# Kernel optimization log

Hardware: AMD Instinct MI355X
Metric: run time of the kernel (lower is better)

Reference implementation:

```python
import jax, jax.numpy as jnp
import numpy as np


def setup_inputs() -> dict:
    key = jax.random.key(0)
    k1, k2, k3 = jax.random.split(key, 3)
    b, n, h, d = 2, 2048, 16, 64
    q = jax.random.normal(k1, (b, n, h, d), dtype=jnp.float32)
    k = jax.random.normal(k2, (b, n, h, d), dtype=jnp.float32)
    v = jax.random.normal(k3, (b, n, h, d), dtype=jnp.float32)
    return {"q": q, "k": k, "v": v, "is_causal": 1}


def reference(q, k, v, is_causal):
    # q, k, v: [b, n, h, d]
    b, n, h, d = q.shape
    scale = 1.0 / jnp.sqrt(jnp.asarray(d, dtype=q.dtype))
    # scores: [b, h, n_q, n_k]
    scores = jnp.einsum("bqhd,bkhd->bhqk", q, k) * scale
    if is_causal:
        causal_mask = jnp.triu(jnp.ones((n, n), dtype=bool), k=1)  # True above diagonal
        scores = jnp.where(causal_mask[None, None, :, :], jnp.asarray(-jnp.inf, scores.dtype), scores)
    attn = jax.nn.softmax(scores, axis=-1)
    # output back to [b, n, h, d]
    out = jnp.einsum("bhqk,bkhd->bqhd", attn, v)
    return out
```

## Files before the change

### kernel.cpp

```cpp
#include <hip/hip_runtime.h>
#include <hip/hip_bf16.h>
#include <math.h>

typedef __bf16 bf16x8 __attribute__((ext_vector_type(8)));
typedef __bf16 bf16x4 __attribute__((ext_vector_type(4)));
typedef __bf16 bf16x2 __attribute__((ext_vector_type(2)));
typedef float  f32x4  __attribute__((ext_vector_type(4)));
typedef float  f32x16 __attribute__((ext_vector_type(16)));
typedef unsigned int u32;
typedef unsigned int u32x4 __attribute__((ext_vector_type(4)));

#define HD   64
#define MNEG (-1e30f)
#define KSW(r, c) ((c) ^ (((r) & 7) << 3))
#define VSW(r, c) ((c) ^ ((((r) >> 2) & 7) << 3))

#define NSLOT   1024
#define ACC_FL  (NSLOT * 8192)
#define ML_FL   (NSLOT * 256)
#define WS_NEED ((size_t)(ACC_FL + ML_FL) * 4)

static __device__ __forceinline__ u32 pkbf(float a, float b) {
  bf16x2 t; t[0] = (__bf16)a; t[1] = (__bf16)b;
  return __builtin_bit_cast(u32, t);
}

template <int SPLIT>
__global__ __launch_bounds__(256, 2)
void fattn_fwd(const float* __restrict__ Q, const float* __restrict__ K,
               const float* __restrict__ V, const int* __restrict__ causal_p,
               float* __restrict__ O, float* __restrict__ wsAcc,
               float* __restrict__ wsML, int B, int N, int H) {
  __shared__ alignas(16) __bf16 Kl[2][64][64];
  __shared__ alignas(16) __bf16 Vt[2][64][64];

  const int tid  = threadIdx.x;
  const int wave = tid >> 6;
  const int lane = tid & 63;
  const int l31  = lane & 31;
  const int h    = lane >> 5;
  const int lo16 = lane & 15, hi4 = lane >> 4;

  const int causal = causal_p[0];

  int x, bh, t0, t1, slot = 0;
  if constexpr (SPLIT) {
    bh = (int)blockIdx.x & 31;
    const int xc = (int)blockIdx.x >> 5;
    x = 15 - (xc >> 1);
    const int c = xc & 1;
    const int ntile = causal ? (2 * x + 2) : 32;
    t0 = c * 16;
    t1 = min(t0 + 16, ntile);
    if (t0 >= t1) return;
    slot = (bh * 16 + x) * 2 + c;
  } else {
    x  = 15 - ((int)blockIdx.x >> 5);
    bh = (int)blockIdx.x & 31;
    t0 = 0;
    t1 = causal ? (2 * x + 2) : 32;
  }
  const int bb = bh / H, hh = bh - bb * H;
  const int sN = H * HD;

  const float* Qb = Q + (long)bb * N * sN + hh * HD;
  const float* Kb = K + (long)bb * N * sN + hh * HD;
  const float* Vb = V + (long)bb * N * sN + hh * HD;
  float*       Ob = O + (long)bb * N * sN + hh * HD;

  const int q0w = x * 128 + wave * 32;

  const float qscale = 0.125f * 1.44269504088896340736f;
  bf16x8 aq[4];
  {
    const float* qrow = Qb + (long)(q0w + l31) * sN;
#pragma unroll
    for (int ds = 0; ds < 4; ++ds) {
      f32x4 x0 = *(const f32x4*)(qrow + ds * 16 + h * 8);
      f32x4 x1 = *(const f32x4*)(qrow + ds * 16 + h * 8 + 4);
      bf16x8 a;
#pragma unroll
      for (int j = 0; j < 4; ++j) {
        a[j]     = (__bf16)(x0[j] * qscale);
        a[j + 4] = (__bf16)(x1[j] * qscale);
      }
      aq[ds] = a;
    }
  }

  f32x16 accA, accB;
#pragma unroll
  for (int j = 0; j < 16; ++j) { accA[j] = 0.f; accB[j] = 0.f; }
  float m_run = MNEG, l_run = 0.f;

  f32x4 kreg[4], vreg[4];
  auto issue = [&](int tt) {
    const int k0 = tt * 64;
#pragma unroll
    for (int i = 0; i < 4; ++i) {
      const int fl = tid + i * 256;
      const int r = fl >> 4, c4 = (fl & 15) * 4;
      kreg[i] = *(const f32x4*)(Kb + (long)(k0 + r) * sN + c4);
    }
    const float* vrow = Vb + (long)(k0 + wave * 16 + hi4 * 4) * sN + lo16 * 4;
#pragma unroll
    for (int q = 0; q < 4; ++q) vreg[q] = *(const f32x4*)(vrow + (long)q * sN);
  };
  auto wr = [&](int buf) {
#pragma unroll
    for (int i = 0; i < 4; ++i) {
      const int fl = tid + i * 256;
      const int r = fl >> 4, c4 = (fl & 15) * 4;
      bf16x4 kb;
#pragma unroll
      for (int j = 0; j < 4; ++j) kb[j] = (__bf16)kreg[i][j];
      *(bf16x4*)&Kl[buf][r][KSW(r, c4)] = kb;
    }
    const int kv0 = wave * 16 + hi4 * 4;
#pragma unroll
    for (int j = 0; j < 4; ++j) {
      const int d = lo16 * 4 + j;
      bf16x4 vv;
#pragma unroll
      for (int q = 0; q < 4; ++q) vv[q] = (__bf16)vreg[q][j];
      *(bf16x4*)&Vt[buf][d][VSW(d, kv0)] = vv;
    }
  };

  issue(t0);
  wr(0);
  __syncthreads();

  int pb = 0;
  for (int t = t0; t < t1; ++t) {
    const bool pf = (t + 1 < t1);
    if (pf) issue(t + 1);
    const int k0 = t * 64;

    f32x16 p0, p1;
#pragma unroll
    for (int j = 0; j < 16; ++j) { p0[j] = 0.f; p1[j] = 0.f; }
#pragma unroll
    for (int ds = 0; ds < 4; ++ds) {
      const int cc = ds * 16 + h * 8;
      bf16x8 ka = *(const bf16x8*)&Kl[pb][l31][KSW(l31, cc)];
      p0 = __builtin_amdgcn_mfma_f32_32x32x16_bf16(ka, aq[ds], p0, 0, 0, 0);
      bf16x8 kb2 = *(const bf16x8*)&Kl[pb][32 + l31][KSW(32 + l31, cc)];
      p1 = __builtin_amdgcn_mfma_f32_32x32x16_bf16(kb2, aq[ds], p1, 0, 0, 0);
    }

    if (causal && t >= 2 * x) {
      const int qg = q0w + l31;
#pragma unroll
      for (int reg = 0; reg < 16; ++reg) {
        const int crow = (reg & 3) + 8 * (reg >> 2) + 4 * h;
        if (k0 + crow > qg)      p0[reg] = MNEG;
        if (k0 + 32 + crow > qg) p1[reg] = MNEG;
      }
    }

    float t8[8];
#pragma unroll
    for (int j = 0; j < 8; ++j)
      t8[j] = fmaxf(fmaxf(p0[j], p0[j + 8]), fmaxf(p1[j], p1[j + 8]));
#pragma unroll
    for (int stp = 4; stp > 0; stp >>= 1)
#pragma unroll
      for (int j = 0; j < stp; ++j) t8[j] = fmaxf(t8[j], t8[j + stp]);
    const float mx = fmaxf(t8[0], __shfl_xor(t8[0], 32));
    if (!__all(mx - m_run <= 8.0f)) {
      const float mnew = fmaxf(m_run, mx);
      const float fac  = exp2f(m_run - mnew);
      l_run *= fac;
      m_run = mnew;
#pragma unroll
      for (int j = 0; j < 16; ++j) { accA[j] *= fac; accB[j] *= fac; }
    }
#pragma unroll
    for (int j = 0; j < 16; ++j) {
      p0[j] = exp2f(p0[j] - m_run);
      p1[j] = exp2f(p1[j] - m_run);
    }
    float s8[8];
#pragma unroll
    for (int j = 0; j < 8; ++j)
      s8[j] = (p0[j] + p0[j + 8]) + (p1[j] + p1[j + 8]);
#pragma unroll
    for (int stp = 4; stp > 0; stp >>= 1)
#pragma unroll
      for (int j = 0; j < stp; ++j) s8[j] += s8[j + stp];
    const float ps = s8[0] + __shfl_xor(s8[0], 32);
    l_run += ps;

    u32 W0[8], W1[8];
#pragma unroll
    for (int tt = 0; tt < 8; ++tt) {
      W0[tt] = pkbf(p0[2 * tt], p0[2 * tt + 1]);
      W1[tt] = pkbf(p1[2 * tt], p1[2 * tt + 1]);
    }
    auto mkpair = [&](u32 wa, u32 wb, u32& dlo, u32& dhi) {
      const u32 gsel = h ? wa : wb;
      const u32 f = (u32)__shfl_xor((int)gsel, 32);
      dlo = h ? f : wa;
      dhi = h ? wb : f;
    };
    bf16x8 pa[4];
    {
      u32 d0, d1, d2, d3;
      mkpair(W0[0], W0[2], d0, d2); mkpair(W0[1], W0[3], d1, d3);
      pa[0] = __builtin_bit_cast(bf16x8, (u32x4){d0, d1, d2, d3});
      mkpair(W0[4], W0[6], d0, d2); mkpair(W0[5], W0[7], d1, d3);
      pa[1] = __builtin_bit_cast(bf16x8, (u32x4){d0, d1, d2, d3});
      mkpair(W1[0], W1[2], d0, d2); mkpair(W1[1], W1[3], d1, d3);
      pa[2] = __builtin_bit_cast(bf16x8, (u32x4){d0, d1, d2, d3});
      mkpair(W1[4], W1[6], d0, d2); mkpair(W1[5], W1[7], d1, d3);
      pa[3] = __builtin_bit_cast(bf16x8, (u32x4){d0, d1, d2, d3});
    }

#pragma unroll
    for (int ks = 0; ks < 4; ++ks) {
      bf16x8 va = *(const bf16x8*)&Vt[pb][l31][VSW(l31, ks * 16 + h * 8)];
      accA = __builtin_amdgcn_mfma_f32_32x32x16_bf16(va, pa[ks], accA, 0, 0, 0);
    }
#pragma unroll
    for (int ks = 0; ks < 4; ++ks) {
      bf16x8 va = *(const bf16x8*)&Vt[pb][32 + l31][VSW(32 + l31, ks * 16 + h * 8)];
      accB = __builtin_amdgcn_mfma_f32_32x32x16_bf16(va, pa[ks], accB, 0, 0, 0);
    }

    if (pf) wr(pb ^ 1);
    __syncthreads();
    pb ^= 1;
  }

  const int qrel = wave * 32 + l31;
  if constexpr (SPLIT) {
    float* ap = wsAcc + (long)slot * 8192 + qrel * 64;
#pragma unroll
    for (int g = 0; g < 4; ++g) {
      f32x4 o0, o1;
#pragma unroll
      for (int j = 0; j < 4; ++j) { o0[j] = accA[4 * g + j]; o1[j] = accB[4 * g + j]; }
      *(f32x4*)(ap + 8 * g + 4 * h) = o0;
      *(f32x4*)(ap + 32 + 8 * g + 4 * h) = o1;
    }
    if (h == 0) {
      wsML[slot * 256 + qrel] = m_run;
      wsML[slot * 256 + 128 + qrel] = l_run;
    }
  } else {
    const float linv = 1.0f / l_run;
    float* orow = Ob + (long)(q0w + l31) * sN;
#pragma unroll
    for (int g = 0; g < 4; ++g) {
      f32x4 o0, o1;
#pragma unroll
      for (int j = 0; j < 4; ++j) {
        o0[j] = accA[4 * g + j] * linv;
        o1[j] = accB[4 * g + j] * linv;
      }
      *(f32x4*)(orow + 8 * g + 4 * h) = o0;
      *(f32x4*)(orow + 32 + 8 * g + 4 * h) = o1;
    }
  }
}

__global__ __launch_bounds__(256)
void fmerge(const float* __restrict__ wsAcc, const float* __restrict__ wsML,
            const int* __restrict__ causal_p, float* __restrict__ O,
            int B, int N, int H) {
  const int tid = threadIdx.x;
  const int bh = (int)blockIdx.x >> 4;
  const int x  = (int)blockIdx.x & 15;
  const int bb = bh / H, hh = bh - bb * H;
  const int causal = causal_p[0];
  const int ntile = causal ? (2 * x + 2) : 32;
  const int q  = tid >> 1;
  const int dh = (tid & 1) * 32;
  const int slot0 = (bh * 16 + x) * 2;
  const bool v1 = (16 < ntile);

  const float m0 = wsML[slot0 * 256 + q];
  const float l0 = wsML[slot0 * 256 + 128 + q];
  const float m1 = v1 ? wsML[(slot0 + 1) * 256 + q] : MNEG;
  const float l1 = v1 ? wsML[(slot0 + 1) * 256 + 128 + q] : 0.f;
  const float M  = fmaxf(m0, m1);
  const float e0 = exp2f(m0 - M);
  const float e1 = v1 ? exp2f(m1 - M) : 0.f;
  const float inv = 1.0f / (e0 * l0 + e1 * l1);
  const float f0 = e0 * inv, f1 = e1 * inv;

  const float* a0 = wsAcc + (long)slot0 * 8192 + q * 64 + dh;
  const float* a1 = a0 + 8192;
  float* op = O + ((long)(bb * N + x * 128 + q) * H + hh) * HD + dh;
#pragma unroll
  for (int j = 0; j < 8; ++j) {
    f32x4 r0 = *(const f32x4*)(a0 + 4 * j);
    f32x4 o;
#pragma unroll
    for (int e = 0; e < 4; ++e) o[e] = r0[e] * f0;
    if (v1) {
      f32x4 r1 = *(const f32x4*)(a1 + 4 * j);
#pragma unroll
      for (int e = 0; e < 4; ++e) o[e] += r1[e] * f1;
    }
    *(f32x4*)(op + 4 * j) = o;
  }
}

extern "C" void kernel_launch(void* const* d_in, const int* in_sizes, int n_in,
                              void* d_out, int out_size, void* d_ws, size_t ws_size,
                              hipStream_t stream) {
  const float* q = (const float*)d_in[0];
  const float* k = (const float*)d_in[1];
  const float* v = (const float*)d_in[2];
  const int* causal = (const int*)d_in[3];
  float* out = (float*)d_out;
  const int B = 2, N = 2048, H = 16;
  if (ws_size >= WS_NEED) {
    float* wsAcc = (float*)d_ws;
    float* wsML  = wsAcc + ACC_FL;
    fattn_fwd<1><<<dim3(NSLOT), dim3(256), 0, stream>>>(q, k, v, causal, out,
                                                        wsAcc, wsML, B, N, H);
    fmerge<<<dim3(512), dim3(256), 0, stream>>>(wsAcc, wsML, causal, out, B, N, H);
  } else {
    fattn_fwd<0><<<dim3(512), dim3(256), 0, stream>>>(q, k, v, causal, out,
                                                      nullptr, nullptr, B, N, H);
  }
}
```

Baseline: 162.2 us.

## Fuse split-KV merge into attention kernel via atomic counters, reorder and raise occupancy

Removes the separate merge kernel. The last-arriving split block, detected with an atomic counter per query tile, merges both partial results and writes the output directly. Query tiles that need only one chunk now write the output straight away, skipping the workspace round trip. Other changes in the same commit: a lookup table reorders block scheduling to pair long and short chunks, launch bounds rise to 4 blocks per SM, the MFMA sections are wrapped in s_setprio, and exp2f is replaced by the hardware exp2 builtin. The cost is a memset launch for the counters, extra fences, and possible register spilling under the tighter occupancy bound.

```diff
diff --git a/kernel.cpp b/kernel.cpp
--- a/kernel.cpp
+++ b/kernel.cpp
@@ -15,10 +15,24 @@
 #define KSW(r, c) ((c) ^ (((r) & 7) << 3))
 #define VSW(r, c) ((c) ^ ((((r) >> 2) & 7) << 3))
 
-#define NSLOT   1024
-#define ACC_FL  (NSLOT * 8192)
-#define ML_FL   (NSLOT * 256)
-#define WS_NEED ((size_t)(ACC_FL + ML_FL) * 4)
+#if __has_builtin(__builtin_amdgcn_exp2f)
+#define EXP2(x) __builtin_amdgcn_exp2f(x)
+#else
+#define EXP2(x) exp2f(x)
+#endif
+
+#define NSLOT    1024
+#define ACC_FL   (NSLOT * 8192)
+#define ML_FL    (NSLOT * 256)
+#define NCTR     512
+#define WS_NEED  ((size_t)(ACC_FL + ML_FL) * 4 + NCTR * 4)
+
+static __device__ const signed char ORD_X[32] =
+  {15,15,14,13,12,11,10,9,8,7, 14,6, 13,5, 12,4, 11,3, 10,2, 9,1, 8,0,
+   7,6,5,4,3,2,1,0};
+static __device__ const signed char ORD_C[32] =
+  {0,1,0,0,0,0,0,0,0,0, 1,0, 1,0, 1,0, 1,0, 1,0, 1,0, 1,0,
+   1,1,1,1,1,1,1,1};
 
 static __device__ __forceinline__ u32 pkbf(float a, float b) {
   bf16x2 t; t[0] = (__bf16)a; t[1] = (__bf16)b;
@@ -26,13 +40,15 @@
 }
 
 template <int SPLIT>
-__global__ __launch_bounds__(256, 2)
+__global__ __launch_bounds__(256, 4)
 void fattn_fwd(const float* __restrict__ Q, const float* __restrict__ K,
                const float* __restrict__ V, const int* __restrict__ causal_p,
                float* __restrict__ O, float* __restrict__ wsAcc,
-               float* __restrict__ wsML, int B, int N, int H) {
+               float* __restrict__ wsML, int* __restrict__ ctr,
+               int B, int N, int H) {
   __shared__ alignas(16) __bf16 Kl[2][64][64];
   __shared__ alignas(16) __bf16 Vt[2][64][64];
+  __shared__ int s_old;
 
   const int tid  = threadIdx.x;
   const int wave = tid >> 6;
@@ -43,16 +59,17 @@
 
   const int causal = causal_p[0];
 
-  int x, bh, t0, t1, slot = 0;
+  int x, bh, t0, t1, slot = 0, nch = 1;
   if constexpr (SPLIT) {
     bh = (int)blockIdx.x & 31;
-    const int xc = (int)blockIdx.x >> 5;
-    x = 15 - (xc >> 1);
-    const int c = xc & 1;
+    const int idx = (int)blockIdx.x >> 5;
+    x = ORD_X[idx];
+    const int c = ORD_C[idx];
     const int ntile = causal ? (2 * x + 2) : 32;
     t0 = c * 16;
     t1 = min(t0 + 16, ntile);
     if (t0 >= t1) return;
+    nch  = (ntile > 16) ? 2 : 1;
     slot = (bh * 16 + x) * 2 + c;
   } else {
     x  = 15 - ((int)blockIdx.x >> 5);
@@ -140,6 +157,7 @@
     f32x16 p0, p1;
 #pragma unroll
     for (int j = 0; j < 16; ++j) { p0[j] = 0.f; p1[j] = 0.f; }
+    __builtin_amdgcn_s_setprio(1);
 #pragma unroll
     for (int ds = 0; ds < 4; ++ds) {
       const int cc = ds * 16 + h * 8;
@@ -148,6 +166,7 @@
       bf16x8 kb2 = *(const bf16x8*)&Kl[pb][32 + l31][KSW(32 + l31, cc)];
       p1 = __builtin_amdgcn_mfma_f32_32x32x16_bf16(kb2, aq[ds], p1, 0, 0, 0);
     }
+    __builtin_amdgcn_s_setprio(0);
 
     if (causal && t >= 2 * x) {
       const int qg = q0w + l31;
@@ -170,7 +189,7 @@
     const float mx = fmaxf(t8[0], __shfl_xor(t8[0], 32));
     if (!__all(mx - m_run <= 8.0f)) {
       const float mnew = fmaxf(m_run, mx);
-      const float fac  = exp2f(m_run - mnew);
+      const float fac  = EXP2(m_run - mnew);
       l_run *= fac;
       m_run = mnew;
 #pragma unroll
@@ -178,8 +197,8 @@
     }
 #pragma unroll
     for (int j = 0; j < 16; ++j) {
-      p0[j] = exp2f(p0[j] - m_run);
-      p1[j] = exp2f(p1[j] - m_run);
+      p0[j] = EXP2(p0[j] - m_run);
+      p1[j] = EXP2(p1[j] - m_run);
     }
     float s8[8];
 #pragma unroll
@@ -217,6 +236,7 @@
       pa[3] = __builtin_bit_cast(bf16x8, (u32x4){d0, d1, d2, d3});
     }
 
+    __builtin_amdgcn_s_setprio(1);
 #pragma unroll
     for (int ks = 0; ks < 4; ++ks) {
       bf16x8 va = *(const bf16x8*)&Vt[pb][l31][VSW(l31, ks * 16 + h * 8)];
@@ -227,6 +247,7 @@
       bf16x8 va = *(const bf16x8*)&Vt[pb][32 + l31][VSW(32 + l31, ks * 16 + h * 8)];
       accB = __builtin_amdgcn_mfma_f32_32x32x16_bf16(va, pa[ks], accB, 0, 0, 0);
     }
+    __builtin_amdgcn_s_setprio(0);
 
     if (pf) wr(pb ^ 1);
     __syncthreads();
@@ -234,7 +255,7 @@
   }
 
   const int qrel = wave * 32 + l31;
-  if constexpr (SPLIT) {
+  if (SPLIT && nch == 2) {
     float* ap = wsAcc + (long)slot * 8192 + qrel * 64;
 #pragma unroll
     for (int g = 0; g < 4; ++g) {
@@ -247,6 +268,34 @@
     if (h == 0) {
       wsML[slot * 256 + qrel] = m_run;
       wsML[slot * 256 + 128 + qrel] = l_run;
+    }
+    __threadfence();
+    if (tid == 0) s_old = atomicAdd(&ctr[bh * 16 + x], 1);
+    __syncthreads();
+    if (s_old == 0) return;
+    __threadfence();
+    const int oslot = slot ^ 1;
+    const float mo  = wsML[oslot * 256 + qrel];
+    const float lo_ = wsML[oslot * 256 + 128 + qrel];
+    const float M   = fmaxf(m_run, mo);
+    const float e0  = EXP2(m_run - M);
+    const float e1  = EXP2(mo - M);
+    const float inv = 1.0f / (l_run * e0 + lo_ * e1);
+    const float f0 = e0 * inv, f1 = e1 * inv;
+    const float* bp = wsAcc + (long)oslot * 8192 + qrel * 64;
+    float* orow = Ob + (long)(q0w + l31) * sN;
+#pragma unroll
+    for (int g = 0; g < 4; ++g) {
+      f32x4 r0 = *(const f32x4*)(bp + 8 * g + 4 * h);
+      f32x4 r1 = *(const f32x4*)(bp + 32 + 8 * g + 4 * h);
+      f32x4 o0, o1;
+#pragma unroll
+      for (int j = 0; j < 4; ++j) {
+        o0[j] = accA[4 * g + j] * f0 + r0[j] * f1;
+        o1[j] = accB[4 * g + j] * f0 + r1[j] * f1;
+      }
+      *(f32x4*)(orow + 8 * g + 4 * h) = o0;
+      *(f32x4*)(orow + 32 + 8 * g + 4 * h) = o1;
     }
   } else {
     const float linv = 1.0f / l_run;
@@ -262,49 +311,6 @@
       *(f32x4*)(orow + 8 * g + 4 * h) = o0;
       *(f32x4*)(orow + 32 + 8 * g + 4 * h) = o1;
     }
-  }
-}
-
-__global__ __launch_bounds__(256)
-void fmerge(const float* __restrict__ wsAcc, const float* __restrict__ wsML,
-            const int* __restrict__ causal_p, float* __restrict__ O,
-            int B, int N, int H) {
-  const int tid = threadIdx.x;
-  const int bh = (int)blockIdx.x >> 4;
-  const int x  = (int)blockIdx.x & 15;
-  const int bb = bh / H, hh = bh - bb * H;
-  const int causal = causal_p[0];
-  const int ntile = causal ? (2 * x + 2) : 32;
-  const int q  = tid >> 1;
-  const int dh = (tid & 1) * 32;
-  const int slot0 = (bh * 16 + x) * 2;
-  const bool v1 = (16 < ntile);
-
-  const float m0 = wsML[slot0 * 256 + q];
-  const float l0 = wsML[slot0 * 256 + 128 + q];
-  const float m1 = v1 ? wsML[(slot0 + 1) * 256 + q] : MNEG;
-  const float l1 = v1 ? wsML[(slot0 + 1) * 256 + 128 + q] : 0.f;
-  const float M  = fmaxf(m0, m1);
-  const float e0 = exp2f(m0 - M);
-  const float e1 = v1 ? exp2f(m1 - M) : 0.f;
-  const float inv = 1.0f / (e0 * l0 + e1 * l1);
-  const float f0 = e0 * inv, f1 = e1 * inv;
-
-  const float* a0 = wsAcc + (long)slot0 * 8192 + q * 64 + dh;
-  const float* a1 = a0 + 8192;
-  float* op = O + ((long)(bb * N + x * 128 + q) * H + hh) * HD + dh;
-#pragma unroll
-  for (int j = 0; j < 8; ++j) {
-    f32x4 r0 = *(const f32x4*)(a0 + 4 * j);
-    f32x4 o;
-#pragma unroll
-    for (int e = 0; e < 4; ++e) o[e] = r0[e] * f0;
-    if (v1) {
-      f32x4 r1 = *(const f32x4*)(a1 + 4 * j);
-#pragma unroll
-      for (int e = 0; e < 4; ++e) o[e] += r1[e] * f1;
-    }
-    *(f32x4*)(op + 4 * j) = o;
   }
 }
 
@@ -320,11 +326,13 @@
   if (ws_size >= WS_NEED) {
     float* wsAcc = (float*)d_ws;
     float* wsML  = wsAcc + ACC_FL;
-    fattn_fwd<1><<<dim3(NSLOT), dim3(256), 0, stream>>>(q, k, v, causal, out,
-                                                        wsAcc, wsML, B, N, H);
-    fmerge<<<dim3(512), dim3(256), 0, stream>>>(wsAcc, wsML, causal, out, B, N, H);
+    int*   ctr   = (int*)(wsML + ML_FL);
+    hipMemsetAsync(ctr, 0, NCTR * sizeof(int), stream);
+    fattn_fwd<1><<<dim3(1024), dim3(256), 0, stream>>>(q, k, v, causal, out,
+                                                       wsAcc, wsML, ctr, B, N, H);
   } else {
     fattn_fwd<0><<<dim3(512), dim3(256), 0, stream>>>(q, k, v, causal, out,
-                                                      nullptr, nullptr, B, N, H);
+                                                      nullptr, nullptr, nullptr,
+                                                      B, N, H);
   }
 }
```

Result: slower. 303.0 us (+86.9%).
